# Kernel optimization log

Measured on AMD Instinct MI355X. Metric: run time of the kernel, lower is better.

The kernel has to match this reference:

```python
import jax, jax.numpy as jnp
import numpy as np

B, CIN, H, W = 32, 16, 32, 128
COUT = 128


def _run_direction(x_hwbc, p):
    # x_hwbc: (H, W, B, CIN); scan order is raster (top-to-bottom, left-to-right).
    # Predecessors: dim0 = cell above (previous row), dim1 = cell to the left.
    xi = jnp.einsum('hwbc,oc->hwbo', x_hwbc, p['w_ii'])
    xf = jnp.einsum('hwbc,oc->hwbo', x_hwbc, p['w_if'])
    xg = jnp.einsum('hwbc,oc->hwbo', x_hwbc, p['w_ig'])
    xo = jnp.einsum('hwbc,oc->hwbo', x_hwbc, p['w_io'])
    Wdim, Bdim = x_hwbc.shape[1], x_hwbc.shape[2]
    O = p['w_hi'].shape[0]
    ws0, ws1 = p['ws'][0], p['ws'][1]

    def branch(xi_, xf_, xg_, xo_, c, h):
        i = jax.nn.sigmoid(xi_ + h @ p['w_hi'].T + p['b_i'])
        f = jax.nn.sigmoid(xf_ + h @ p['w_hf'].T + p['b_f'])
        g = jnp.tanh(xg_ + h @ p['w_hg'].T + p['b_g'])
        o = jax.nn.sigmoid(xo_ + h @ p['w_ho'].T + p['b_o'])
        cn = f * c + i * g
        return cn, o * jnp.tanh(cn)

    def col_step(carry, inp):
        c_left, h_left = carry                      # (B, O)
        xi_, xf_, xg_, xo_, c_top, h_top = inp      # each (B, O)
        c0, h0 = branch(xi_, xf_, xg_, xo_, c_top, h_top)   # vertical predecessor
        c1, h1 = branch(xi_, xf_, xg_, xo_, c_left, h_left) # horizontal predecessor
        ct = ws0 * c0 + ws1 * c1 + p['bias']
        ht = ws0 * h0 + ws1 * h1 + p['bias']
        return (ct, ht), (ct, ht)

    def row_step(carry, row):
        c_top, h_top = carry                        # (W, B, O)
        xi_r, xf_r, xg_r, xo_r = row
        z = jnp.zeros((Bdim, O), xi_r.dtype)
        _, (c_row, h_row) = jax.lax.scan(col_step, (z, z), (xi_r, xf_r, xg_r, xo_r, c_top, h_top))
        return (c_row, h_row), h_row

    z_row = jnp.zeros((Wdim, Bdim, O), x_hwbc.dtype)
    _, h_all = jax.lax.scan(row_step, (z_row, z_row), (xi, xf, xg, xo))
    return h_all  # (H, W, B, O)


def _forward(x, w_ii, w_hi, b_i, w_if, w_hf, b_f, w_ig, w_hg, b_g,
             w_io, w_ho, b_o, weighted_sum, bias):
    # Four scan directions realized by flipping the grid (lr_tb, rl_tb, lr_bt, rl_bt).
    x_hwbc = jnp.transpose(x, (2, 3, 0, 1))  # (H, W, B, CIN)
    flips = [(False, False), (False, True), (True, False), (True, True)]
    outs = []
    for d, (fy, fx) in enumerate(flips):
        xd = x_hwbc
        if fy:
            xd = xd[::-1]
        if fx:
            xd = xd[:, ::-1]
        p = {'w_ii': w_ii[d], 'w_hi': w_hi[d], 'b_i': b_i[d],
             'w_if': w_if[d], 'w_hf': w_hf[d], 'b_f': b_f[d],
             'w_ig': w_ig[d], 'w_hg': w_hg[d], 'b_g': b_g[d],
             'w_io': w_io[d], 'w_ho': w_ho[d], 'b_o': b_o[d],
             'ws': weighted_sum[d], 'bias': bias[d]}
        h = _run_direction(xd, p)
        if fy:
            h = h[::-1]
        if fx:
            h = h[:, ::-1]
        outs.append(h)
    h4 = jnp.stack(outs)                      # (4, H, W, B, O)
    return jnp.transpose(h4, (0, 4, 3, 1, 2)) # (4, O, B, H, W)


def setup_inputs() -> dict:
    key = jax.random.key(0)
    ks = jax.random.split(key, 16)
    xw = lambda k: jax.random.normal(k, (4, COUT, CIN), jnp.float32) * 0.05
    hw = lambda k: jax.random.normal(k, (4, COUT, COUT), jnp.float32) * 0.05
    bb = lambda k: jax.random.normal(k, (4, COUT), jnp.float32) * 0.05
    return {
        'x': jax.random.normal(ks[0], (B, CIN, H, W), jnp.float32),
        'w_ii': xw(ks[1]), 'w_hi': hw(ks[2]), 'b_i': bb(ks[3]),
        'w_if': xw(ks[4]), 'w_hf': hw(ks[5]), 'b_f': bb(ks[6]),
        'w_ig': xw(ks[7]), 'w_hg': hw(ks[8]), 'b_g': bb(ks[9]),
        'w_io': xw(ks[10]), 'w_ho': hw(ks[11]), 'b_o': bb(ks[12]),
        'weighted_sum': jax.random.uniform(ks[13], (4, 2), jnp.float32),
        'bias': bb(ks[14]),
    }


def reference(x, w_ii, w_hi, b_i, w_if, w_hf, b_f, w_ig, w_hg, b_g,
              w_io, w_ho, b_o, weighted_sum, bias):
    return _forward(x, w_ii, w_hi, b_i, w_if, w_hf, b_f, w_ig, w_hg, b_g,
                    w_io, w_ho, b_o, weighted_sum, bias)
```

## Files before the change

kernel.cpp:

```cpp
#include <hip/hip_runtime.h>

#define Hh 32
#define Ww 128
#define BB 32
#define CC 16
#define OO 128
#define SPIN_CAP (1 << 23)
#define FSTRIDE 32

typedef __attribute__((ext_vector_type(8))) short short8;
typedef __attribute__((ext_vector_type(4))) float f32x4;

__device__ inline short f2bf(float f) {
    unsigned u = __builtin_bit_cast(unsigned, f);
    unsigned r = (u + 0x7FFFu + ((u >> 16) & 1u)) >> 16;
    return (short)r;
}
__device__ inline float bf2f(short s) {
    unsigned u = ((unsigned)(unsigned short)s) << 16;
    return __builtin_bit_cast(float, u);
}
__device__ inline float rcp_(float x) { return __builtin_amdgcn_rcpf(x); }
__device__ inline float sigm(float x) {
    return rcp_(1.f + __builtin_amdgcn_exp2f(-1.442695041f * x));
}
__device__ inline float tanh_(float x) {
    return 1.f - 2.f * rcp_(__builtin_amdgcn_exp2f(2.885390082f * x) + 1.f);
}

__device__ inline unsigned long long aload64(const unsigned long long* p) {
    return __hip_atomic_load(p, __ATOMIC_RELAXED, __HIP_MEMORY_SCOPE_AGENT);
}
__device__ inline void astore64(unsigned long long* p, unsigned long long v) {
    __hip_atomic_store(p, v, __ATOMIC_RELAXED, __HIP_MEMORY_SCOPE_AGENT);
}
__device__ inline void astore16(short* p, short v) {
    __hip_atomic_store(p, v, __ATOMIC_RELAXED, __HIP_MEMORY_SCOPE_AGENT);
}
__device__ inline int aloadI(const int* p) {
    return __hip_atomic_load(p, __ATOMIC_RELAXED, __HIP_MEMORY_SCOPE_AGENT);
}
__device__ inline void astoreI(int* p, int v) {
    __hip_atomic_store(p, v, __ATOMIC_RELAXED, __HIP_MEMORY_SCOPE_AGENT);
}

__global__ void mdlstm_init(const float* __restrict__ x, short* __restrict__ xT,
                            int* __restrict__ flags) {
    int idx = blockIdx.x * 256 + threadIdx.x;
    if (blockIdx.x < 64) flags[idx] = 0;
    int w = idx & 127;
    int h = (idx >> 7) & 31;
    int c = (idx >> 12) & 15;
    int b = idx >> 16;
    float v = x[idx];
    xT[((h * Ww + w) * BB + b) * CC + c] = f2bf(v);
}

__global__ void __launch_bounds__(512, 1) mdlstm_main(
    const short* __restrict__ xT,
    const float* __restrict__ w_ii, const float* __restrict__ w_hi, const float* __restrict__ b_i,
    const float* __restrict__ w_if, const float* __restrict__ w_hf, const float* __restrict__ b_f,
    const float* __restrict__ w_ig, const float* __restrict__ w_hg, const float* __restrict__ b_g,
    const float* __restrict__ w_io, const float* __restrict__ w_ho, const float* __restrict__ b_o,
    const float* __restrict__ wsum, const float* __restrict__ bias,
    short* __restrict__ hring, float* __restrict__ cring,
    int* __restrict__ prog, int* __restrict__ cons,
    float* __restrict__ out, int depth)
{
    const int chain = blockIdx.x & 7;
    const int r     = blockIdx.x >> 3;
    const int d     = chain >> 1;
    const int s     = chain & 1;
    const int b0    = s * 16;
    const bool fy   = (d >= 2);
    const bool fx   = (d & 1);
    const int hh    = fy ? (Hh - 1 - r) : r;

    const int tid  = threadIdx.x;
    const int wv   = tid >> 6;
    const int lane = tid & 63;
    const int lr   = lane & 15;
    const int lh   = lane >> 4;
    const int on   = wv * 16 + lr;

    __shared__ short stage[16 * 16 * 128];

    const float* whp[4] = {w_hi, w_hf, w_hg, w_ho};
    const float* wip[4] = {w_ii, w_if, w_ig, w_io};
    short8 whf[4][4];
    short8 wif_[4];
#pragma unroll
    for (int g = 0; g < 4; ++g) {
#pragma unroll
        for (int kt = 0; kt < 4; ++kt) {
            const float* p = whp[g] + ((d * OO + on) * OO + kt * 32 + lh * 8);
            short8 f;
#pragma unroll
            for (int j = 0; j < 8; ++j) f[j] = f2bf(p[j]);
            whf[g][kt] = f;
        }
        short8 fi = (short8)(short)0;
        if (lh < 2) {
            const float* p = wip[g] + ((d * OO + on) * CC + lh * 8);
#pragma unroll
            for (int j = 0; j < 8; ++j) fi[j] = f2bf(p[j]);
        }
        wif_[g] = fi;
    }

    const float bi  = b_i[d * OO + on];
    const float bf_ = b_f[d * OO + on];
    const float bg_ = b_g[d * OO + on];
    const float bo_ = b_o[d * OO + on];
    const float bb_ = bias[d * OO + on];
    const float ws0 = wsum[d * 2 + 0];
    const float ws1 = wsum[d * 2 + 1];

    int* topf      = prog + ((d * 32 + (r - 1)) * 2 + s) * FSTRIDE;
    int* myprog    = prog + ((d * 32 + r) * 2 + s) * FSTRIDE;
    int* mycons    = cons + ((d * 32 + r) * 2 + s) * FSTRIDE;
    int* consnext  = cons + ((d * 32 + (r + 1)) * 2 + s) * FSTRIDE;

    const int rbh_me  = ((d * 32 + r)     * 2 + s) * depth * (16 * OO);
    const int rbh_top = ((d * 32 + (r-1)) * 2 + s) * depth * (16 * OO);
    const int rbc_me  = ((d * 32 + r)     * 2 + s) * depth * (OO * 16);
    const int rbc_top = ((d * 32 + (r-1)) * 2 + s) * depth * (OO * 16);
    const int smask   = depth - 1;

    short8 hLf[4];
#pragma unroll
    for (int kt = 0; kt < 4; ++kt) hLf[kt] = (short8)(short)0;
    float cL[4] = {0.f, 0.f, 0.f, 0.f};

    float c0A[4], h0A[4], c0B[4], h0B[4];
#pragma unroll
    for (int j = 0; j < 4; ++j) { c0A[j] = h0A[j] = c0B[j] = h0B[j] = 0.f; }
    f32x4 axB[4];

    int top_seen = 0, cons_seen = 0;
    const f32x4 zacc = {0.f, 0.f, 0.f, 0.f};

    short8 xfA = (short8)(short)0, xfB = (short8)(short)0;
    short8 xfN0 = (short8)(short)0, xfN1 = (short8)(short)0;
    if (lh < 2) {
        const int w0 = fx ? (Ww - 1) : 0;
        const int w1 = fx ? (Ww - 2) : 1;
        xfA = *(const short8*)(xT + ((hh * Ww + w0) * BB + b0 + lr) * CC + lh * 8);
        xfB = *(const short8*)(xT + ((hh * Ww + w1) * BB + b0 + lr) * CC + lh * 8);
    }

#pragma unroll 2
    for (int wsc = 0; wsc < Ww; ++wsc) {
        const int ww    = fx ? (Ww - 1 - wsc) : wsc;
        const int slot  = wsc & smask;
        const int wslot = ww & 15;
        const bool evenc = ((wsc & 1) == 0);

        if (evenc) {
            short8 hTfA[4], hTfB[4];
            float cTA[4], cTB[4];
            if (r > 0) {
                const int need = wsc + 2;
                if (top_seen < need) {
                    int spin = 0;
                    while (top_seen < need && spin < SPIN_CAP) {
                        const int v = aloadI(topf);
                        if (v < need) { __builtin_amdgcn_s_sleep(1); ++spin; } else top_seen = v;
                    }
                }
                const short* hb = hring + rbh_top + slot * (16 * OO) + lr * OO;
                const short* hb2 = hb + 16 * OO;
#pragma unroll
                for (int kt = 0; kt < 4; ++kt) {
                    union { unsigned long long q[2]; short8 v; } w;
                    w.q[0] = aload64((const unsigned long long*)(hb + kt * 32 + lh * 8));
                    w.q[1] = aload64((const unsigned long long*)(hb + kt * 32 + lh * 8 + 4));
                    hTfA[kt] = w.v;
                }
#pragma unroll
                for (int kt = 0; kt < 4; ++kt) {
                    union { unsigned long long q[2]; short8 v; } w;
                    w.q[0] = aload64((const unsigned long long*)(hb2 + kt * 32 + lh * 8));
                    w.q[1] = aload64((const unsigned long long*)(hb2 + kt * 32 + lh * 8 + 4));
                    hTfB[kt] = w.v;
                }
                const unsigned long long* cp =
                    (const unsigned long long*)(cring + rbc_top + slot * (OO * 16) + on * 16 + lh * 4);
                union { unsigned long long q; float f[2]; } c01, c23;
                c01.q = aload64(cp);
                c23.q = aload64(cp + 1);
                cTA[0] = c01.f[0]; cTA[1] = c01.f[1]; cTA[2] = c23.f[0]; cTA[3] = c23.f[1];
                const unsigned long long* cpB =
                    (const unsigned long long*)(cring + rbc_top + (slot + 1) * (OO * 16) + on * 16 + lh * 4);
                c01.q = aload64(cpB);
                c23.q = aload64(cpB + 1);
                cTB[0] = c01.f[0]; cTB[1] = c01.f[1]; cTB[2] = c23.f[0]; cTB[3] = c23.f[1];
            } else {
#pragma unroll
                for (int kt = 0; kt < 4; ++kt) { hTfA[kt] = (short8)(short)0; hTfB[kt] = (short8)(short)0; }
#pragma unroll
                for (int j = 0; j < 4; ++j) { cTA[j] = 0.f; cTB[j] = 0.f; }
            }

            f32x4 axA[4];
#pragma unroll
            for (int g = 0; g < 4; ++g) {
                axA[g] = __builtin_amdgcn_mfma_f32_16x16x32_bf16(xfA, wif_[g], zacc, 0, 0, 0);
                axB[g] = __builtin_amdgcn_mfma_f32_16x16x32_bf16(xfB, wif_[g], zacc, 0, 0, 0);
            }

            if (lh < 2 && wsc + 3 < Ww + 1) {
                if (wsc + 2 < Ww) {
                    const int wN0 = fx ? (Ww - 3 - wsc) : (wsc + 2);
                    xfN0 = *(const short8*)(xT + ((hh * Ww + wN0) * BB + b0 + lr) * CC + lh * 8);
                }
                if (wsc + 3 < Ww) {
                    const int wN1 = fx ? (Ww - 4 - wsc) : (wsc + 3);
                    xfN1 = *(const short8*)(xT + ((hh * Ww + wN1) * BB + b0 + lr) * CC + lh * 8);
                }
            }

            {
                f32x4 aT[4];
#pragma unroll
                for (int g = 0; g < 4; ++g) {
                    f32x4 a = axA[g];
#pragma unroll
                    for (int kt = 0; kt < 4; ++kt)
                        a = __builtin_amdgcn_mfma_f32_16x16x32_bf16(hTfA[kt], whf[g][kt], a, 0, 0, 0);
                    aT[g] = a;
                }
#pragma unroll
                for (int j = 0; j < 4; ++j) {
                    float iT = sigm(aT[0][j] + bi);
                    float fT = sigm(aT[1][j] + bf_);
                    float gT = tanh_(aT[2][j] + bg_);
                    float oT = sigm(aT[3][j] + bo_);
                    float c0 = fT * cTA[j] + iT * gT;
                    c0A[j] = c0;
                    h0A[j] = oT * tanh_(c0);
                }
            }
            {
                f32x4 aT[4];
#pragma unroll
                for (int g = 0; g < 4; ++g) {
                    f32x4 a = axB[g];
#pragma unroll
                    for (int kt = 0; kt < 4; ++kt)
                        a = __builtin_amdgcn_mfma_f32_16x16x32_bf16(hTfB[kt], whf[g][kt], a, 0, 0, 0);
                    aT[g] = a;
                }
#pragma unroll
                for (int j = 0; j < 4; ++j) {
                    float iT = sigm(aT[0][j] + bi);
                    float fT = sigm(aT[1][j] + bf_);
                    float gT = tanh_(aT[2][j] + bg_);
                    float oT = sigm(aT[3][j] + bo_);
                    float c0 = fT * cTB[j] + iT * gT;
                    c0B[j] = c0;
                    h0B[j] = oT * tanh_(c0);
                }
            }
        }

        f32x4 accL[4];
        {
#pragma unroll
            for (int g = 0; g < 4; ++g) {
                f32x4 a = evenc
                    ? __builtin_amdgcn_mfma_f32_16x16x32_bf16(xfA, wif_[g], zacc, 0, 0, 0)
                    : axB[g];
#pragma unroll
                for (int kt = 0; kt < 4; ++kt)
                    a = __builtin_amdgcn_mfma_f32_16x16x32_bf16(hLf[kt], whf[g][kt], a, 0, 0, 0);
                accL[g] = a;
            }
        }

        float ctv[4];
        union { short sh[4]; unsigned long long q; } hpack;
#pragma unroll
        for (int j = 0; j < 4; ++j) {
            float iL = sigm(accL[0][j] + bi);
            float fL = sigm(accL[1][j] + bf_);
            float gL = tanh_(accL[2][j] + bg_);
            float oL = sigm(accL[3][j] + bo_);
            float c1 = fL * cL[j] + iL * gL;
            float h1 = oL * tanh_(c1);

            const float c0 = evenc ? c0A[j] : c0B[j];
            const float h0 = evenc ? h0A[j] : h0B[j];
            float ct = ws0 * c0 + ws1 * c1 + bb_;
            float ht = ws0 * h0 + ws1 * h1 + bb_;
            cL[j] = ct;
            ctv[j] = ct;
            hpack.sh[j] = f2bf(ht);
        }

        if ((wsc & 15) == 0 && wsc != 0) __syncthreads();

#pragma unroll
        for (int j = 0; j < 4; ++j) {
            const int b = lh * 4 + j;
            stage[wslot * 2048 + b * 128 + ((((on >> 3) ^ b) << 3)) + (on & 7)] = hpack.sh[j];
        }

        if (r < 31 && evenc && wsc >= depth) {
            const int need = wsc - (depth - 2);
            if (cons_seen < need) {
                int spin = 0;
                while (cons_seen < need && spin < SPIN_CAP) {
                    const int v = aloadI(consnext);
                    if (v < need) { __builtin_amdgcn_s_sleep(1); ++spin; } else cons_seen = v;
                }
            }
        }

        if (r < 31) {
            short* hp = hring + rbh_me + slot * (16 * OO) + on;
#pragma unroll
            for (int j = 0; j < 4; ++j)
                astore16(hp + (lh * 4 + j) * OO, hpack.sh[j]);
            union { float f[2]; unsigned long long q; } p01, p23;
            p01.f[0] = ctv[0]; p01.f[1] = ctv[1];
            p23.f[0] = ctv[2]; p23.f[1] = ctv[3];
            unsigned long long* cp =
                (unsigned long long*)(cring + rbc_me + slot * (OO * 16) + on * 16 + lh * 4);
            astore64(cp, p01.q);
            astore64(cp + 1, p23.q);
        }

        __syncthreads();

        if (!evenc && tid == 0) {
            if (r < 31) astoreI(myprog, wsc + 1);
            if (r > 0)  astoreI(mycons, wsc + 1);
        }

        if (r > 0 && !evenc && wsc < Ww - 1) {
            const int v = aloadI(topf);
            if (v > top_seen) top_seen = v;
        }

#pragma unroll
        for (int kt = 0; kt < 4; ++kt) {
            const int idx = wslot * 2048 + lr * 128 + ((((kt << 2) + lh) ^ lr) << 3);
            hLf[kt] = *(const short8*)&stage[idx];
        }

        if (!evenc) { xfA = xfN0; xfB = xfN1; }

        if ((wsc & 15) == 15) {
            const int wbase = ww & ~15;
            const int q  = tid & 3;
            const int r0 = tid >> 2;
#pragma unroll
            for (int i = 0; i < 16; ++i) {
                const int row = r0 + (i << 7);
                const int o = row >> 4;
                const int b = row & 15;
                f32x4 v;
#pragma unroll
                for (int k = 0; k < 4; ++k)
                    v[k] = bf2f(stage[(q * 4 + k) * 2048 + b * 128
                                      + (((o >> 3) ^ b) << 3) + (o & 7)]);
                float* op = out + ((size_t)((d * OO + o) * BB + b0 + b)) * (Hh * Ww)
                                + hh * Ww + wbase + q * 4;
                __builtin_nontemporal_store(v, (f32x4*)op);
            }
        }
    }
}

extern "C" void kernel_launch(void* const* d_in, const int* in_sizes, int n_in,
                              void* d_out, int out_size, void* d_ws, size_t ws_size,
                              hipStream_t stream) {
    (void)in_sizes; (void)n_in; (void)out_size;

    const float* x     = (const float*)d_in[0];
    const float* w_ii  = (const float*)d_in[1];
    const float* w_hi  = (const float*)d_in[2];
    const float* b_i   = (const float*)d_in[3];
    const float* w_if  = (const float*)d_in[4];
    const float* w_hf  = (const float*)d_in[5];
    const float* b_f   = (const float*)d_in[6];
    const float* w_ig  = (const float*)d_in[7];
    const float* w_hg  = (const float*)d_in[8];
    const float* b_g   = (const float*)d_in[9];
    const float* w_io  = (const float*)d_in[10];
    const float* w_ho  = (const float*)d_in[11];
    const float* b_o   = (const float*)d_in[12];
    const float* wsum  = (const float*)d_in[13];
    const float* bias  = (const float*)d_in[14];
    float* outp        = (float*)d_out;

    char* ws = (char*)d_ws;
    int*   flags  = (int*)ws;
    short* xTp    = (short*)(ws + (64u << 10));
    const size_t off_h = (64u << 10) + (4u << 20);

    int depth = 8;
    const size_t need8 = off_h + ((size_t)8 << 20) + ((size_t)16 << 20) + (1u << 20);
    if (ws_size < need8) depth = 4;

    short* hringp = (short*)(ws + off_h);
    float* cringp = (float*)(ws + off_h + ((size_t)depth << 20));
    int*   progp  = flags;
    int*   consp  = flags + 256 * FSTRIDE;

    hipLaunchKernelGGL(mdlstm_init, dim3(8192), dim3(256), 0, stream, x, xTp, flags);

    mdlstm_main<<<dim3(256), dim3(512), 0, stream>>>(
        xTp,
        w_ii, w_hi, b_i,
        w_if, w_hf, b_f,
        w_ig, w_hg, b_g,
        w_io, w_ho, b_o,
        wsum, bias,
        hringp, cringp, progp, consp,
        outp, depth);
}
```

Before: 1.027 ms.

## Use per-wave progress flags and lighter LDS-only barriers in wavefront pipeline

Each wave now publishes its own progress and consumer flag (indexed by wave id) after waiting only for its own outstanding global stores. Consumers check all eight per-wave flags with a ballot instead of a single flag written by thread 0 after a full barrier. Block-wide __syncthreads is replaced by an LDS-count wait plus s_barrier, so the global-store drain no longer sits on the critical path of every step. The x-projection for the even column is also reused from axA instead of being recomputed. The trade-off is more flag traffic per check and a reliance on subtle memory-ordering assumptions for the relaxed atomic stores.

```diff
diff --git a/kernel.cpp b/kernel.cpp
--- a/kernel.cpp
+++ b/kernel.cpp
@@ -42,6 +42,20 @@
 }
 __device__ inline void astoreI(int* p, int v) {
     __hip_atomic_store(p, v, __ATOMIC_RELAXED, __HIP_MEMORY_SCOPE_AGENT);
+}
+
+__device__ inline void wait_vm0() {
+    asm volatile("s_waitcnt vmcnt(0)" ::: "memory");
+}
+__device__ inline void bar_lds() {
+    asm volatile("s_waitcnt lgkmcnt(0)" ::: "memory");
+    __builtin_amdgcn_s_barrier();
+    asm volatile("" ::: "memory");
+}
+
+__device__ inline bool flags_ge(const int* pf, int lane, int need) {
+    const int v = aloadI(pf + (lane & 7));
+    return __ballot(v >= need) == ~0ull;
 }
 
 __global__ void mdlstm_init(const float* __restrict__ x, short* __restrict__ xT,
@@ -135,7 +149,9 @@
     float c0A[4], h0A[4], c0B[4], h0B[4];
 #pragma unroll
     for (int j = 0; j < 4; ++j) { c0A[j] = h0A[j] = c0B[j] = h0B[j] = 0.f; }
-    f32x4 axB[4];
+    f32x4 axA[4], axB[4];
+#pragma unroll
+    for (int g = 0; g < 4; ++g) { axA[g] = (f32x4){0,0,0,0}; axB[g] = (f32x4){0,0,0,0}; }
 
     int top_seen = 0, cons_seen = 0;
     const f32x4 zacc = {0.f, 0.f, 0.f, 0.f};
@@ -164,11 +180,11 @@
                 if (top_seen < need) {
                     int spin = 0;
                     while (top_seen < need && spin < SPIN_CAP) {
-                        const int v = aloadI(topf);
-                        if (v < need) { __builtin_amdgcn_s_sleep(1); ++spin; } else top_seen = v;
+                        if (flags_ge(topf, lane, need)) top_seen = need;
+                        else { __builtin_amdgcn_s_sleep(1); ++spin; }
                     }
                 }
-                const short* hb = hring + rbh_top + slot * (16 * OO) + lr * OO;
+                const short* hb  = hring + rbh_top + slot * (16 * OO) + lr * OO;
                 const short* hb2 = hb + 16 * OO;
 #pragma unroll
                 for (int kt = 0; kt < 4; ++kt) {
@@ -202,14 +218,13 @@
                 for (int j = 0; j < 4; ++j) { cTA[j] = 0.f; cTB[j] = 0.f; }
             }
 
-            f32x4 axA[4];
 #pragma unroll
             for (int g = 0; g < 4; ++g) {
                 axA[g] = __builtin_amdgcn_mfma_f32_16x16x32_bf16(xfA, wif_[g], zacc, 0, 0, 0);
                 axB[g] = __builtin_amdgcn_mfma_f32_16x16x32_bf16(xfB, wif_[g], zacc, 0, 0, 0);
             }
 
-            if (lh < 2 && wsc + 3 < Ww + 1) {
+            if (lh < 2) {
                 if (wsc + 2 < Ww) {
                     const int wN0 = fx ? (Ww - 3 - wsc) : (wsc + 2);
                     xfN0 = *(const short8*)(xT + ((hh * Ww + wN0) * BB + b0 + lr) * CC + lh * 8);
@@ -265,17 +280,13 @@
         }
 
         f32x4 accL[4];
-        {
-#pragma unroll
-            for (int g = 0; g < 4; ++g) {
-                f32x4 a = evenc
-                    ? __builtin_amdgcn_mfma_f32_16x16x32_bf16(xfA, wif_[g], zacc, 0, 0, 0)
-                    : axB[g];
-#pragma unroll
-                for (int kt = 0; kt < 4; ++kt)
-                    a = __builtin_amdgcn_mfma_f32_16x16x32_bf16(hLf[kt], whf[g][kt], a, 0, 0, 0);
-                accL[g] = a;
-            }
+#pragma unroll
+        for (int g = 0; g < 4; ++g) {
+            f32x4 a = evenc ? axA[g] : axB[g];
+#pragma unroll
+            for (int kt = 0; kt < 4; ++kt)
+                a = __builtin_amdgcn_mfma_f32_16x16x32_bf16(hLf[kt], whf[g][kt], a, 0, 0, 0);
+            accL[g] = a;
         }
 
         float ctv[4];
@@ -298,7 +309,7 @@
             hpack.sh[j] = f2bf(ht);
         }
 
-        if ((wsc & 15) == 0 && wsc != 0) __syncthreads();
+        if ((wsc & 15) == 0 && wsc != 0) bar_lds();
 
 #pragma unroll
         for (int j = 0; j < 4; ++j) {
@@ -311,8 +322,8 @@
             if (cons_seen < need) {
                 int spin = 0;
                 while (cons_seen < need && spin < SPIN_CAP) {
-                    const int v = aloadI(consnext);
-                    if (v < need) { __builtin_amdgcn_s_sleep(1); ++spin; } else cons_seen = v;
+                    if (flags_ge(consnext, lane, need)) cons_seen = need;
+                    else { __builtin_amdgcn_s_sleep(1); ++spin; }
                 }
             }
         }
@@ -331,16 +342,18 @@
             astore64(cp + 1, p23.q);
         }
 
-        __syncthreads();
-
-        if (!evenc && tid == 0) {
-            if (r < 31) astoreI(myprog, wsc + 1);
-            if (r > 0)  astoreI(mycons, wsc + 1);
-        }
+        if (!evenc) {
+            if (r < 31) wait_vm0();
+            if (lane == 0) {
+                if (r < 31) astoreI(myprog + wv, wsc + 1);
+                if (r > 0)  astoreI(mycons + wv, wsc + 1);
+            }
+        }
+
+        bar_lds();
 
         if (r > 0 && !evenc && wsc < Ww - 1) {
-            const int v = aloadI(topf);
-            if (v > top_seen) top_seen = v;
+            if (flags_ge(topf, lane, wsc + 3)) top_seen = wsc + 3;
         }
 
 #pragma unroll
```

After: 1.230 ms. 1.2x slower.
